# Kernel optimization log

Hardware: AMD Instinct MI355X
Metric: run time of the kernel (lower is better)

Reference implementation:

```python
import jax, jax.numpy as jnp
import numpy as np

N, L, S, C, H = 4, 2048, 4096, 256, 8
D = C // H          # head dim = 32
HID = 4 * C         # mlp hidden = 1024
LN_EPS = 1e-5
LA_EPS = 1e-6


def _layer_norm(x, g, b):
    m = x.mean(-1, keepdims=True)
    v = ((x - m) ** 2).mean(-1, keepdims=True)
    return (x - m) * jax.lax.rsqrt(v + LN_EPS) * g + b


def _linear_attention(q, k, v):
    # q: [N,L,H,D], k/v: [N,S,H,D]  (elu feature map linear attention)
    Q = jax.nn.elu(q) + 1.0
    K = jax.nn.elu(k) + 1.0
    v_len = v.shape[1]
    KV = jnp.einsum('nshd,nshv->nhdv', K, v / v_len)
    Z = 1.0 / (jnp.einsum('nlhd,nhd->nlh', Q, K.sum(axis=1)) + LA_EPS)
    return jnp.einsum('nlhd,nhdv,nlh->nlhv', Q, KV, Z) * v_len


def setup_inputs() -> dict:
    key = jax.random.key(0)
    ks = jax.random.split(key, 32)
    f32 = jnp.float32
    w = lambda k, *s: (jax.random.normal(k, s, dtype=f32) * 0.02)
    inp = {
        'tgt': jax.random.normal(ks[0], (N, L, C), dtype=f32),
        'memory': jax.random.normal(ks[1], (N, S, C), dtype=f32),
        'tgt_pos': jax.random.normal(ks[2], (N, L, C), dtype=f32),
        'pos_embed': w(ks[3], 1, S, C),
        # layer norms
        'ln1_g': jnp.ones((C,), f32), 'ln1_b': jnp.zeros((C,), f32),
        'ln2_g': jnp.ones((C,), f32), 'ln2_b': jnp.zeros((C,), f32),
        'ln3_g': jnp.ones((C,), f32), 'ln3_b': jnp.zeros((C,), f32),
        # self-attn projections (stored (in,out))
        'wq': w(ks[4], C, C), 'bq': jnp.zeros((C,), f32),
        'wk': w(ks[5], C, C), 'bk': jnp.zeros((C,), f32),
        'wv': w(ks[6], C, C), 'bv': jnp.zeros((C,), f32),
        'w_merge': w(ks[7], C, C),
        # cross-attn (CCAttention) projections
        'cwq': w(ks[8], C, C), 'cbq': jnp.zeros((C,), f32),
        'cwk': w(ks[9], C, C), 'cbk': jnp.zeros((C,), f32),
        'cwv': w(ks[10], C, C), 'cbv': jnp.zeros((C,), f32),
        'cwo': w(ks[11], C, C), 'cbo': jnp.zeros((C,), f32),
        # mlp (fc1 -> dwconv3x3 -> gelu -> fc2)
        'mw1': w(ks[12], C, HID), 'mb1': jnp.zeros((HID,), f32),
        'dw_k': w(ks[13], HID, 1, 3, 3), 'dw_b': jnp.zeros((HID,), f32),
        'mw2': w(ks[14], HID, C), 'mb2': jnp.zeros((C,), f32),
        'num_points': L,
    }
    return inp


def reference(tgt, memory, tgt_pos, pos_embed,
              ln1_g, ln1_b, ln2_g, ln2_b, ln3_g, ln3_b,
              wq, bq, wk, bk, wv, bv, w_merge,
              cwq, cbq, cwk, cbk, cwv, cbv, cwo, cbo,
              mw1, mb1, dw_k, dw_b, mw2, mb2, num_points):
    n, l, c = tgt.shape
    # ---- self attention (linear attention) ----
    tgt2 = _layer_norm(tgt, ln1_g, ln1_b)
    qk = tgt2 + tgt_pos
    q = (qk @ wq + bq).reshape(n, l, H, D)
    k = (qk @ wk + bk).reshape(n, l, H, D)
    v = (tgt2 @ wv + bv).reshape(n, l, H, D)
    msg = _linear_attention(q, k, v).reshape(n, l, c) @ w_merge
    tgt = tgt + msg  # dropout is identity in eval
    # ---- cross attention (CCAttention, softmax MHA) ----
    tgt2 = _layer_norm(tgt, ln2_g, ln2_b)
    mem = memory + pos_embed
    cq = (tgt2 @ cwq + cbq).reshape(n, l, H, D)
    ck = (mem @ cwk + cbk).reshape(n, -1, H, D)
    cv = (mem @ cwv + cbv).reshape(n, -1, H, D)
    scale = D ** -0.5
    attn = jax.nn.softmax(jnp.einsum('nlhd,nshd->nhls', cq, ck) * scale, axis=-1)
    cmsg = jnp.einsum('nhls,nshd->nlhd', attn, cv).reshape(n, l, c) @ cwo + cbo
    tgt = tgt + cmsg
    # ---- MLP with depthwise conv over (num_points, 1) grid ----
    x = _layer_norm(tgt, ln3_g, ln3_b)
    h = x @ mw1 + mb1                                   # [n,l,HID]
    hi = h.transpose(0, 2, 1).reshape(n, HID, num_points, 1)
    hi = jax.lax.conv_general_dilated(
        hi, dw_k, window_strides=(1, 1), padding=((1, 1), (1, 1)),
        feature_group_count=HID,
        dimension_numbers=('NCHW', 'OIHW', 'NCHW'))
    hi = hi + dw_b[None, :, None, None]
    h = hi.reshape(n, HID, l).transpose(0, 2, 1)
    h = jax.nn.gelu(h, approximate=False)
    mlp_out = h @ mw2 + mb2
    return tgt + mlp_out
```

## Files before the change

kernel.cpp:

```cpp
#include <hip/hip_runtime.h>
#include <hip/hip_bf16.h>
#include <math.h>

#define NB 4
#define LL 2048
#define SS 4096
#define CC 256
#define HH 8
#define DD 32
#define HIDN 1024
#define NSPLIT 2

using bf16 = __hip_bfloat16;
typedef __attribute__((ext_vector_type(8))) short short8;
typedef __attribute__((ext_vector_type(4))) short short4v;
typedef __attribute__((ext_vector_type(4))) float floatx4;

__device__ __forceinline__ float b2f(bf16 x) { return __bfloat162float(x); }
__device__ __forceinline__ short f2bs(float x) {
    bf16 h = __float2bfloat16(x);
    return *(short*)&h;
}
__device__ __forceinline__ short f2bs_fast(float x) {
    return (short)(__float_as_uint(x) >> 16);
}
__device__ __forceinline__ float s2f(short s) {
    bf16 h = *(bf16*)&s;
    return __bfloat162float(h);
}

#if __has_builtin(__builtin_amdgcn_exp2f)
#define EXP2(x) __builtin_amdgcn_exp2f(x)
#else
#define EXP2(x) exp2f(x)
#endif

__device__ __forceinline__ bool probe_f32(const unsigned* p) {
    return p[0] == 0x3F800000u;
}
__device__ __forceinline__ float ldx(const void* p, size_t i, bool f32m) {
    return f32m ? ((const float*)p)[i] : b2f(((const bf16*)p)[i]);
}

__global__ __launch_bounds__(256)
void zero_kernel(float* __restrict__ p, int n) {
    int i = blockIdx.x * 256 + threadIdx.x;
    if (i < n) p[i] = 0.0f;
}

struct WPack { const void* p[10]; };

__global__ __launch_bounds__(256)
void wprep_kernel(WPack pk, short* __restrict__ dst,
                  const unsigned* __restrict__ probe) {
    const bool f32m = probe_f32(probe);
    const int z = blockIdx.z;
    const int K = (z == 9) ? 1024 : 256;
    const int N = (z == 8) ? 1024 : 256;
    const size_t off = (z < 8) ? (size_t)z * 65536 : (z == 8 ? 524288u : 786432u);
    const int k0 = blockIdx.y * 64, n0 = blockIdx.x * 64;
    if (k0 >= K || n0 >= N) return;
    __shared__ float T[64][65];
    const void* src = pk.p[z];
    const int tid = threadIdx.x;
    #pragma unroll
    for (int p = 0; p < 16; ++p) {
        int idx = tid + p * 256;
        int r = idx >> 6, c = idx & 63;
        T[r][c] = ldx(src, (size_t)(k0 + r) * N + n0 + c, f32m);
    }
    __syncthreads();
    short* d = dst + off;
    #pragma unroll
    for (int p = 0; p < 16; ++p) {
        int idx = tid + p * 256;
        int c2 = idx >> 6, r2 = idx & 63;
        d[(size_t)(n0 + c2) * K + k0 + r2] = f2bs(T[r2][c2]);
    }
}

__global__ __launch_bounds__(256)
void ln_kernel(const void* __restrict__ xr, const float* __restrict__ xf,
               const void* __restrict__ g, const void* __restrict__ bta,
               const void* __restrict__ pos,
               short* __restrict__ y, short* __restrict__ y2,
               const unsigned* __restrict__ probe) {
    const bool f32m = probe_f32(probe);
    const int row = blockIdx.x;
    const int c = threadIdx.x;
    const size_t base = (size_t)row * CC;
    float x = xr ? ldx(xr, base + c, f32m) : xf[base + c];
    float a = x, b = x * x;
    #pragma unroll
    for (int off = 32; off; off >>= 1) {
        a += __shfl_down(a, off);
        b += __shfl_down(b, off);
    }
    __shared__ float sa[4], sb[4];
    if ((c & 63) == 0) { sa[c >> 6] = a; sb[c >> 6] = b; }
    __syncthreads();
    float s1 = sa[0] + sa[1] + sa[2] + sa[3];
    float s2 = sb[0] + sb[1] + sb[2] + sb[3];
    float mean = s1 * (1.0f / CC);
    float var = s2 * (1.0f / CC) - mean * mean;
    float inv = rsqrtf(var + 1e-5f);
    float yv = (x - mean) * inv * ldx(g, c, f32m) + ldx(bta, c, f32m);
    y[base + c] = f2bs(yv);
    if (y2) y2[base + c] = f2bs(yv + ldx(pos, base + c, f32m));
}

__global__ __launch_bounds__(256)
void addpos_kernel(const void* __restrict__ mem, const void* __restrict__ pos,
                   short* __restrict__ out, const unsigned* __restrict__ probe) {
    const bool f32m = probe_f32(probe);
    const int row = blockIdx.x;
    const int c = threadIdx.x;
    const int s = row & (SS - 1);
    out[(size_t)row * CC + c] =
        f2bs(ldx(mem, (size_t)row * CC + c, f32m) + ldx(pos, (size_t)s * CC + c, f32m));
}

template <int BM, int BN, int EPI, int OUTMODE, int TRANSC2>
__global__ __launch_bounds__(256)
void gemm_mfma_kernel(const short* __restrict__ A, const short* __restrict__ Bt,
                      const void* __restrict__ bias, const void* __restrict__ bias2,
                      const float* __restrict__ residF, const void* __restrict__ residR,
                      void* __restrict__ Cout, void* __restrict__ Cout2,
                      int M, int N, int K, const unsigned* __restrict__ probe) {
    const bool f32m = probe_f32(probe);
    constexpr int WM = BM / 2, AI = WM / 16;
    constexpr int WN = BN / 2, BJ = WN / 16;
    constexpr int ACH = (BM == 128) ? 4 : 2;
    constexpr int BCH = (BN == 128) ? 4 : 2;
    __shared__ __attribute__((aligned(16))) short As[BM][72];
    __shared__ __attribute__((aligned(16))) short Bs[BN][72];
    const int tid = threadIdx.x;
    const int ln = tid & 15, quad = (tid >> 4) & 3, w = tid >> 6;
    const int wm = (w & 1) * WM, wn = (w >> 1) * WN;
    const int bm = blockIdx.y * BM, bn = blockIdx.x * BN;
    const int ar = (BM == 128) ? (tid >> 1) : (tid >> 2);
    const int ac = (BM == 128) ? ((tid & 1) * 32) : ((tid & 3) * 16);
    const int br = (BN == 128) ? (tid >> 1) : (tid >> 2);
    const int bc = (BN == 128) ? ((tid & 1) * 32) : ((tid & 3) * 16);

    short8 pa[ACH], pb[BCH];
    {
        const short* ag = &A[(size_t)(bm + ar) * K + ac];
        #pragma unroll
        for (int t = 0; t < ACH; ++t) pa[t] = *(const short8*)(ag + t * 8);
        const short* bg = &Bt[(size_t)(bn + br) * K + bc];
        #pragma unroll
        for (int t = 0; t < BCH; ++t) pb[t] = *(const short8*)(bg + t * 8);
    }
    floatx4 acc[AI][BJ] = {};
    for (int k0 = 0; k0 < K; k0 += 64) {
        #pragma unroll
        for (int t = 0; t < ACH; ++t) *(short8*)&As[ar][ac + t * 8] = pa[t];
        #pragma unroll
        for (int t = 0; t < BCH; ++t) *(short8*)&Bs[br][bc + t * 8] = pb[t];
        if (k0 + 64 < K) {
            const short* ag = &A[(size_t)(bm + ar) * K + k0 + 64 + ac];
            #pragma unroll
            for (int t = 0; t < ACH; ++t) pa[t] = *(const short8*)(ag + t * 8);
            const short* bg = &Bt[(size_t)(bn + br) * K + k0 + 64 + bc];
            #pragma unroll
            for (int t = 0; t < BCH; ++t) pb[t] = *(const short8*)(bg + t * 8);
        }
        __syncthreads();
        #pragma unroll
        for (int ks = 0; ks < 2; ++ks) {
            short8 af[AI], bf[BJ];
            #pragma unroll
            for (int i = 0; i < AI; ++i)
                af[i] = *(const short8*)&As[wm + i * 16 + ln][ks * 32 + quad * 8];
            #pragma unroll
            for (int j = 0; j < BJ; ++j)
                bf[j] = *(const short8*)&Bs[wn + j * 16 + ln][ks * 32 + quad * 8];
            #pragma unroll
            for (int i = 0; i < AI; ++i)
                #pragma unroll
                for (int j = 0; j < BJ; ++j)
                    acc[i][j] = __builtin_amdgcn_mfma_f32_16x16x32_bf16(af[i], bf[j], acc[i][j], 0, 0, 0);
        }
        __syncthreads();
    }
    #pragma unroll
    for (int i = 0; i < AI; ++i)
        #pragma unroll
        for (int j = 0; j < BJ; ++j) {
            const int gr0 = bm + wm + i * 16 + quad * 4;
            const int gc = bn + wn + j * 16 + ln;
            const bool hi = (Cout2 != nullptr) && (gc >= 256);
            const int col = hi ? gc - 256 : gc;
            const int sN = Cout2 ? 256 : N;
            void* co = hi ? Cout2 : Cout;
            const void* bb = hi ? bias2 : bias;
            float vv[4];
            #pragma unroll
            for (int r = 0; r < 4; ++r) {
                float v = acc[i][j][r];
                if (bb) v += ldx(bb, col, f32m);
                if (EPI == 1) v = (v > 0.0f) ? (v + 1.0f) : __expf(v);
                const size_t o = (size_t)(gr0 + r) * sN + col;
                if (residF) v += residF[o];
                if (residR) v += ldx(residR, o, f32m);
                vv[r] = v;
            }
            if (TRANSC2 && hi) {
                const int nb = gr0 >> 12;
                const int s = gr0 & (SS - 1);
                short4v pk4 = {f2bs(vv[0]), f2bs(vv[1]), f2bs(vv[2]), f2bs(vv[3])};
                *(short4v*)&((short*)co)[((size_t)nb * CC + col) * SS + s] = pk4;
            } else {
                #pragma unroll
                for (int r = 0; r < 4; ++r) {
                    const size_t o = (size_t)(gr0 + r) * sN + col;
                    if (OUTMODE == 0) ((float*)co)[o] = vv[r];
                    else if (OUTMODE == 2) ((short*)co)[o] = f2bs(vv[r]);
                    else {
                        if (f32m) ((float*)co)[o] = vv[r];
                        else      ((bf16*)co)[o] = __float2bfloat16(vv[r]);
                    }
                }
            }
        }
}

#define KVSPLIT 16
__global__ __launch_bounds__(256)
void linattn_kv_kernel(const float* __restrict__ Kp, const float* __restrict__ Vp,
                       float* __restrict__ KV, float* __restrict__ Ksum) {
    const int h = blockIdx.x, n = blockIdx.y, z = blockIdx.z;
    __shared__ __attribute__((aligned(16))) float Kt[64][33];
    __shared__ __attribute__((aligned(16))) float Vt[64][32];
    const int tid = threadIdx.x;
    const int d = tid >> 3, e0 = (tid & 7) * 4;
    const int sbeg = z * (LL / KVSPLIT), send = sbeg + (LL / KVSPLIT);
    float acc[4] = {}, ks = 0.0f;
    for (int s0 = sbeg; s0 < send; s0 += 64) {
        #pragma unroll
        for (int p = 0; p < 8; ++p) {
            int idx = tid + p * 256;
            int r = idx >> 5, c = idx & 31;
            size_t gaddr = (size_t)((n * LL) + s0 + r) * CC + h * DD + c;
            Kt[r][c] = Kp[gaddr];
            Vt[r][c] = Vp[gaddr];
        }
        __syncthreads();
        for (int s = 0; s < 64; ++s) {
            float kd = Kt[s][d];
            ks += kd;
            float4 v4 = *(const float4*)&Vt[s][e0];
            acc[0] += kd * v4.x; acc[1] += kd * v4.y;
            acc[2] += kd * v4.z; acc[3] += kd * v4.w;
        }
        __syncthreads();
    }
    float* kvp = &KV[(size_t)((n * HH + h) * DD + d) * DD + e0];
    atomicAdd(&kvp[0], acc[0]); atomicAdd(&kvp[1], acc[1]);
    atomicAdd(&kvp[2], acc[2]); atomicAdd(&kvp[3], acc[3]);
    if ((tid & 7) == 0) atomicAdd(&Ksum[(n * HH + h) * DD + d], ks);
}

__global__ __launch_bounds__(256)
void linattn_out_kernel(const float* __restrict__ Qp, const float* __restrict__ KV,
                        const float* __restrict__ Ksum, short* __restrict__ Out) {
    const int lt = blockIdx.x, h = blockIdx.y, n = blockIdx.z;
    __shared__ float KVs[32][33];
    __shared__ float Ks[32];
    __shared__ float Qs[64][33];
    const int tid = threadIdx.x;
    for (int p = 0; p < 4; ++p) {
        int idx = tid + p * 256;
        KVs[idx >> 5][idx & 31] = KV[(size_t)(n * HH + h) * (DD * DD) + idx];
    }
    if (tid < 32) Ks[tid] = Ksum[(n * HH + h) * DD + tid];
    for (int p = 0; p < 8; ++p) {
        int idx = tid + p * 256;
        int r = idx >> 5, c = idx & 31;
        Qs[r][c] = Qp[(size_t)((n * LL) + lt * 64 + r) * CC + h * DD + c];
    }
    __syncthreads();
    const int e = tid & 31;
    for (int ii = 0; ii < 8; ++ii) {
        const int i = (tid >> 5) + ii * 8;
        float num = 0.0f, den = 0.0f;
        for (int d = 0; d < 32; ++d) {
            float q = Qs[i][d];
            num += q * KVs[d][e];
            den += q * Ks[d];
        }
        Out[(size_t)((n * LL) + lt * 64 + i) * CC + h * DD + e] = f2bs(num / (den + 1e-6f));
    }
}

__global__ __launch_bounds__(256)
void flash_mfma_kernel(const short* __restrict__ Q, const short* __restrict__ K,
                       const short* __restrict__ V,
                       float* __restrict__ Of, float* __restrict__ Lp) {
    const int lt = blockIdx.x, h = blockIdx.y;
    const int n = blockIdx.z >> 1, sp = blockIdx.z & 1;
    const int tid = threadIdx.x;
    const int ln = tid & 15;
    const int quad = (tid >> 4) & 3;
    const int w = tid >> 6;
    const int NT = NB * LL;
    const float qscale = 0.17677669529663687f * 1.4426950408889634f;

    __shared__ __attribute__((aligned(16))) short Qs[64][40];
    __shared__ __attribute__((aligned(16))) short Ks[64][40];
    __shared__ __attribute__((aligned(16))) short Vp[32][72];

    {
        const int r = tid >> 2, c0 = (tid & 3) * 8;
        short8 qv = *(const short8*)&Q[(size_t)((n * LL) + lt * 64 + r) * CC + h * DD + c0];
        short tmp[8];
        #pragma unroll
        for (int j = 0; j < 8; ++j) tmp[j] = f2bs(s2f(qv[j]) * qscale);
        *(short8*)&Qs[r][c0] = *(short8*)tmp;
    }
    __syncthreads();

    short8 bQ = *(const short8*)&Qs[w * 16 + ln][quad * 8];

    float l_sum = 0.0f;
    floatx4 o0 = {0.f, 0.f, 0.f, 0.f};
    floatx4 o1 = {0.f, 0.f, 0.f, 0.f};
    const floatx4 zinit = {-24.f, -24.f, -24.f, -24.f};

    const int r_st = tid >> 2, c0_st = (tid & 3) * 8;
    const int e_st = tid >> 3, m_st = tid & 7;
    const int K32 = (m_st >> 2) * 32;
    const int h4 = ((m_st >> 1) & 1) * 4;
    const int q0s = (2 * m_st) & 3;
    const int slotA = K32 + q0s * 8 + h4;
    const int slotB = K32 + (q0s + 1) * 8 + h4;

    const int sbeg = sp * (SS / NSPLIT), send = sbeg + (SS / NSPLIT);
    for (int s0 = sbeg; s0 < send; s0 += 64) {
        *(short8*)&Ks[r_st][c0_st] =
            *(const short8*)&K[(size_t)((n * SS) + s0 + r_st) * CC + h * DD + c0_st];
        {
            short8 vv = *(const short8*)&V[((size_t)n * CC + h * DD + e_st) * SS + s0 + m_st * 8];
            short4v lo = {vv[0], vv[1], vv[2], vv[3]};
            short4v hi = {vv[4], vv[5], vv[6], vv[7]};
            *(short4v*)&Vp[e_st][slotA] = lo;
            *(short4v*)&Vp[e_st][slotB] = hi;
        }
        __syncthreads();

        floatx4 sc[4];
        #pragma unroll
        for (int g = 0; g < 4; ++g) {
            short8 aK = *(const short8*)&Ks[g * 16 + ln][quad * 8];
            sc[g] = __builtin_amdgcn_mfma_f32_16x16x32_bf16(aK, bQ, zinit, 0, 0, 0);
        }

        #pragma unroll
        for (int ks = 0; ks < 2; ++ks) {
            short tmp[8];
            #pragma unroll
            for (int j = 0; j < 8; ++j) {
                float p = EXP2(sc[2 * ks + (j >> 2)][j & 3]);
                l_sum += p;
                tmp[j] = f2bs_fast(p);
            }
            short8 aP = *(short8*)tmp;
            short8 bV0 = *(const short8*)&Vp[ln][ks * 32 + quad * 8];
            short8 bV1 = *(const short8*)&Vp[16 + ln][ks * 32 + quad * 8];
            o0 = __builtin_amdgcn_mfma_f32_16x16x32_bf16(aP, bV0, o0, 0, 0, 0);
            o1 = __builtin_amdgcn_mfma_f32_16x16x32_bf16(aP, bV1, o1, 0, 0, 0);
        }
        __syncthreads();
    }

    float s = l_sum;
    s += __shfl_xor(s, 16);
    s += __shfl_xor(s, 32);
    const int rowbase = lt * 64 + w * 16;
    if (quad == 0)
        Lp[((size_t)sp * NT + (size_t)n * LL + rowbase + ln) * HH + h] = s;
    #pragma unroll
    for (int r = 0; r < 4; ++r) {
        const size_t row = (size_t)n * LL + rowbase + quad * 4 + r;
        float* o = &Of[((size_t)sp * NT + row) * CC + h * DD];
        o[ln] = o0[r];
        o[16 + ln] = o1[r];
    }
}

__global__ __launch_bounds__(256)
void flash_merge_kernel(const float* __restrict__ Of, const float* __restrict__ Lp,
                        short* __restrict__ O) {
    const int row = blockIdx.x, c = threadIdx.x, h = c >> 5;
    const size_t NT = (size_t)NB * LL;
    float l = Lp[(size_t)row * HH + h] + Lp[(NT + row) * HH + h];
    float v = Of[(size_t)row * CC + c] + Of[NT * CC + (size_t)row * CC + c];
    O[(size_t)row * CC + c] = f2bs(v / l);
}

__global__ __launch_bounds__(256)
void dwconv_gelu_kernel(const short* __restrict__ H1, const void* __restrict__ wk,
                        const void* __restrict__ wb, short* __restrict__ H2,
                        const unsigned* __restrict__ probe) {
    const bool f32m = probe_f32(probe);
    const int row = blockIdx.x;
    const int l = row & (LL - 1);
    const int c0 = threadIdx.x * 4;
    const short* cur = &H1[(size_t)row * HIDN + c0];
    short4v xc = *(const short4v*)cur;
    short4v xm = {}, xp = {};
    if (l > 0)      xm = *(const short4v*)(cur - HIDN);
    if (l < LL - 1) xp = *(const short4v*)(cur + HIDN);
    short r[4];
    #pragma unroll
    for (int j = 0; j < 4; ++j) {
        int ch = c0 + j;
        float wm = ldx(wk, ch * 9 + 1, f32m);
        float w0 = ldx(wk, ch * 9 + 4, f32m);
        float wp = ldx(wk, ch * 9 + 7, f32m);
        float v = s2f(xm[j]) * wm + s2f(xc[j]) * w0 + s2f(xp[j]) * wp + ldx(wb, ch, f32m);
        r[j] = f2bs(0.5f * v * (1.0f + erff(v * 0.70710678118654752f)));
    }
    short4v out = {r[0], r[1], r[2], r[3]};
    *(short4v*)&H2[(size_t)row * HIDN + c0] = out;
}

extern "C" void kernel_launch(void* const* d_in, const int* in_sizes, int n_in,
                              void* d_out, int out_size, void* d_ws, size_t ws_size,
                              hipStream_t stream) {
    const void* tgt      = d_in[0];
    const void* memory   = d_in[1];
    const void* tgt_pos  = d_in[2];
    const void* pos_emb  = d_in[3];
    const void* ln1_g = d_in[4],  *ln1_b = d_in[5];
    const void* ln2_g = d_in[6],  *ln2_b = d_in[7];
    const void* ln3_g = d_in[8],  *ln3_b = d_in[9];
    const void* wq = d_in[10], *bq = d_in[11];
    const void* wk = d_in[12], *bk = d_in[13];
    const void* wv = d_in[14], *bv = d_in[15];
    const void* w_merge = d_in[16];
    const void* cwq = d_in[17], *cbq = d_in[18];
    const void* cwk = d_in[19], *cbk = d_in[20];
    const void* cwv = d_in[21], *cbv = d_in[22];
    const void* cwo = d_in[23], *cbo = d_in[24];
    const void* mw1 = d_in[25], *mb1 = d_in[26];
    const void* dw_k = d_in[27], *dw_b = d_in[28];
    const void* mw2 = d_in[29], *mb2 = d_in[30];
    const unsigned* probe = (const unsigned*)d_in[4];

    char* w = (char*)d_ws;
    const size_t MB = 1024 * 1024;
    short* lnout_b = (short*)(w + 0 * MB);
    short* qk_b    = (short*)(w + 4 * MB);
    float* Tbuf    = (float*)(w + 8 * MB);
    float* phiq    = (float*)(w + 16 * MB);
    float* phik    = (float*)(w + 24 * MB);
    float* vbuf    = (float*)(w + 32 * MB);
    float* KVb     = (float*)(w + 40 * MB);
    float* Ksb     = (float*)(w + 40 * MB + 131072);
    short* cqbuf   = (short*)(w + 41 * MB);
    short* membuf  = (short*)(w + 45 * MB);
    short* ckbuf   = (short*)(w + 53 * MB);
    short* cvT     = (short*)(w + 69 * MB);
    short* flashO  = (short*)(w + 77 * MB);
    short* wT      = (short*)(w + 81 * MB);
    float* Ofb     = (float*)(w + 16 * MB);
    float* Lpb     = (float*)(w + 32 * MB);
    short* H1      = (short*)(w + 16 * MB);
    short* H2      = (short*)(w + 32 * MB);

    short* wqT  = wT + 0 * 65536;
    short* wvT  = wT + 2 * 65536;
    short* wmT  = wT + 3 * 65536;
    short* cwqT = wT + 4 * 65536;
    short* cwkT = wT + 5 * 65536;
    short* cwoT = wT + 7 * 65536;
    short* mw1T = wT + 524288;
    short* mw2T = wT + 786432;

    const int NT = NB * LL;
    const int NS = NB * SS;
    const dim3 blk(256);

    WPack pk;
    pk.p[0] = wq;  pk.p[1] = wk;  pk.p[2] = wv;  pk.p[3] = w_merge;
    pk.p[4] = cwq; pk.p[5] = cwk; pk.p[6] = cwv; pk.p[7] = cwo;
    pk.p[8] = mw1; pk.p[9] = mw2;
    wprep_kernel<<<dim3(16, 16, 10), blk, 0, stream>>>(pk, wT, probe);
    zero_kernel<<<dim3(137), blk, 0, stream>>>(KVb, 35072);

    ln_kernel<<<NT, blk, 0, stream>>>(tgt, nullptr, ln1_g, ln1_b, tgt_pos, lnout_b, qk_b, probe);
    gemm_mfma_kernel<64, 64, 1, 0, 0><<<dim3(8, NT / 64), blk, 0, stream>>>(
        qk_b, wqT, bq, bk, nullptr, nullptr, phiq, phik, NT, 512, CC, probe);
    gemm_mfma_kernel<64, 64, 0, 0, 0><<<dim3(4, NT / 64), blk, 0, stream>>>(
        lnout_b, wvT, bv, nullptr, nullptr, nullptr, vbuf, nullptr, NT, CC, CC, probe);
    linattn_kv_kernel<<<dim3(HH, NB, KVSPLIT), blk, 0, stream>>>(phik, vbuf, KVb, Ksb);
    linattn_out_kernel<<<dim3(LL / 64, HH, NB), blk, 0, stream>>>(phiq, KVb, Ksb, (short*)vbuf);
    gemm_mfma_kernel<64, 64, 0, 0, 0><<<dim3(4, NT / 64), blk, 0, stream>>>(
        (short*)vbuf, wmT, nullptr, nullptr, nullptr, tgt, Tbuf, nullptr, NT, CC, CC, probe);

    ln_kernel<<<NT, blk, 0, stream>>>(nullptr, Tbuf, ln2_g, ln2_b, nullptr, lnout_b, nullptr, probe);
    addpos_kernel<<<NS, blk, 0, stream>>>(memory, pos_emb, membuf, probe);
    gemm_mfma_kernel<64, 64, 0, 2, 0><<<dim3(4, NT / 64), blk, 0, stream>>>(
        lnout_b, cwqT, cbq, nullptr, nullptr, nullptr, cqbuf, nullptr, NT, CC, CC, probe);
    gemm_mfma_kernel<64, 64, 0, 2, 1><<<dim3(8, NS / 64), blk, 0, stream>>>(
        membuf, cwkT, cbk, cbv, nullptr, nullptr, ckbuf, cvT, NS, 512, CC, probe);
    flash_mfma_kernel<<<dim3(LL / 64, HH, NB * NSPLIT), blk, 0, stream>>>(
        cqbuf, ckbuf, cvT, Ofb, Lpb);
    flash_merge_kernel<<<NT, blk, 0, stream>>>(Ofb, Lpb, flashO);
    gemm_mfma_kernel<64, 64, 0, 0, 0><<<dim3(4, NT / 64), blk, 0, stream>>>(
        flashO, cwoT, cbo, nullptr, Tbuf, nullptr, Tbuf, nullptr, NT, CC, CC, probe);

    ln_kernel<<<NT, blk, 0, stream>>>(nullptr, Tbuf, ln3_g, ln3_b, nullptr, lnout_b, nullptr, probe);
    gemm_mfma_kernel<64, 64, 0, 2, 0><<<dim3(16, NT / 64), blk, 0, stream>>>(
        lnout_b, mw1T, mb1, nullptr, nullptr, nullptr, H1, nullptr, NT, HIDN, CC, probe);
    dwconv_gelu_kernel<<<NT, blk, 0, stream>>>(H1, dw_k, dw_b, H2, probe);
    gemm_mfma_kernel<64, 64, 0, 1, 0><<<dim3(4, NT / 64), blk, 0, stream>>>(
        H2, mw2T, mb2, nullptr, Tbuf, nullptr, d_out, nullptr, NT, CC, HIDN, probe);

    (void)in_sizes; (void)n_in; (void)out_size; (void)ws_size;
}
```

Measured before the change: 425.4 us.

## Load GEMM tiles straight into LDS with global_load_lds and enlarge tiles

```diff
diff --git a/kernel.cpp b/kernel.cpp
--- a/kernel.cpp
+++ b/kernel.cpp
@@ -34,6 +34,12 @@
 #else
 #define EXP2(x) exp2f(x)
 #endif
+
+__device__ __forceinline__ void gload16(const void* g, void* l) {
+    __builtin_amdgcn_global_load_lds(
+        (const __attribute__((address_space(1))) void*)g,
+        (__attribute__((address_space(3))) void*)l, 16, 0, 0);
+}
 
 __device__ __forceinline__ bool probe_f32(const unsigned* p) {
     return p[0] == 0x3F800000u;
@@ -130,41 +136,26 @@
     const bool f32m = probe_f32(probe);
     constexpr int WM = BM / 2, AI = WM / 16;
     constexpr int WN = BN / 2, BJ = WN / 16;
-    constexpr int ACH = (BM == 128) ? 4 : 2;
-    constexpr int BCH = (BN == 128) ? 4 : 2;
-    __shared__ __attribute__((aligned(16))) short As[BM][72];
-    __shared__ __attribute__((aligned(16))) short Bs[BN][72];
+    __shared__ __attribute__((aligned(16))) short As[BM][64];
+    __shared__ __attribute__((aligned(16))) short Bs[BN][64];
     const int tid = threadIdx.x;
     const int ln = tid & 15, quad = (tid >> 4) & 3, w = tid >> 6;
     const int wm = (w & 1) * WM, wn = (w >> 1) * WN;
     const int bm = blockIdx.y * BM, bn = blockIdx.x * BN;
-    const int ar = (BM == 128) ? (tid >> 1) : (tid >> 2);
-    const int ac = (BM == 128) ? ((tid & 1) * 32) : ((tid & 3) * 16);
-    const int br = (BN == 128) ? (tid >> 1) : (tid >> 2);
-    const int bc = (BN == 128) ? ((tid & 1) * 32) : ((tid & 3) * 16);
-
-    short8 pa[ACH], pb[BCH];
-    {
-        const short* ag = &A[(size_t)(bm + ar) * K + ac];
-        #pragma unroll
-        for (int t = 0; t < ACH; ++t) pa[t] = *(const short8*)(ag + t * 8);
-        const short* bg = &Bt[(size_t)(bn + br) * K + bc];
-        #pragma unroll
-        for (int t = 0; t < BCH; ++t) pb[t] = *(const short8*)(bg + t * 8);
-    }
+    const int l64 = tid & 63;
+    const int srow = l64 >> 3, scol = (l64 & 7) * 8;
+
     floatx4 acc[AI][BJ] = {};
     for (int k0 = 0; k0 < K; k0 += 64) {
         #pragma unroll
-        for (int t = 0; t < ACH; ++t) *(short8*)&As[ar][ac + t * 8] = pa[t];
-        #pragma unroll
-        for (int t = 0; t < BCH; ++t) *(short8*)&Bs[br][bc + t * 8] = pb[t];
-        if (k0 + 64 < K) {
-            const short* ag = &A[(size_t)(bm + ar) * K + k0 + 64 + ac];
-            #pragma unroll
-            for (int t = 0; t < ACH; ++t) pa[t] = *(const short8*)(ag + t * 8);
-            const short* bg = &Bt[(size_t)(bn + br) * K + k0 + 64 + bc];
-            #pragma unroll
-            for (int t = 0; t < BCH; ++t) pb[t] = *(const short8*)(bg + t * 8);
+        for (int t = 0; t < BM / 32; ++t) {
+            const int r = (t * 4 + w) * 8 + srow;
+            gload16(&A[(size_t)(bm + r) * K + k0 + scol], &As[r][scol]);
+        }
+        #pragma unroll
+        for (int t = 0; t < BN / 32; ++t) {
+            const int r = (t * 4 + w) * 8 + srow;
+            gload16(&Bt[(size_t)(bn + r) * K + k0 + scol], &Bs[r][scol]);
         }
         __syncthreads();
         #pragma unroll
@@ -491,7 +482,7 @@
     zero_kernel<<<dim3(137), blk, 0, stream>>>(KVb, 35072);
 
     ln_kernel<<<NT, blk, 0, stream>>>(tgt, nullptr, ln1_g, ln1_b, tgt_pos, lnout_b, qk_b, probe);
-    gemm_mfma_kernel<64, 64, 1, 0, 0><<<dim3(8, NT / 64), blk, 0, stream>>>(
+    gemm_mfma_kernel<128, 64, 1, 0, 0><<<dim3(8, NT / 128), blk, 0, stream>>>(
         qk_b, wqT, bq, bk, nullptr, nullptr, phiq, phik, NT, 512, CC, probe);
     gemm_mfma_kernel<64, 64, 0, 0, 0><<<dim3(4, NT / 64), blk, 0, stream>>>(
         lnout_b, wvT, bv, nullptr, nullptr, nullptr, vbuf, nullptr, NT, CC, CC, probe);
@@ -504,7 +495,7 @@
     addpos_kernel<<<NS, blk, 0, stream>>>(memory, pos_emb, membuf, probe);
     gemm_mfma_kernel<64, 64, 0, 2, 0><<<dim3(4, NT / 64), blk, 0, stream>>>(
         lnout_b, cwqT, cbq, nullptr, nullptr, nullptr, cqbuf, nullptr, NT, CC, CC, probe);
-    gemm_mfma_kernel<64, 64, 0, 2, 1><<<dim3(8, NS / 64), blk, 0, stream>>>(
+    gemm_mfma_kernel<128, 128, 0, 2, 1><<<dim3(4, NS / 128), blk, 0, stream>>>(
         membuf, cwkT, cbk, cbv, nullptr, nullptr, ckbuf, cvT, NS, 512, CC, probe);
     flash_mfma_kernel<<<dim3(LL / 64, HH, NB * NSPLIT), blk, 0, stream>>>(
         cqbuf, ckbuf, cvT, Ofb, Lpb);
@@ -513,7 +504,7 @@
         flashO, cwoT, cbo, nullptr, Tbuf, nullptr, Tbuf, nullptr, NT, CC, CC, probe);
 
     ln_kernel<<<NT, blk, 0, stream>>>(nullptr, Tbuf, ln3_g, ln3_b, nullptr, lnout_b, nullptr, probe);
-    gemm_mfma_kernel<64, 64, 0, 2, 0><<<dim3(16, NT / 64), blk, 0, stream>>>(
+    gemm_mfma_kernel<128, 128, 0, 2, 0><<<dim3(8, NT / 128), blk, 0, stream>>>(
         lnout_b, mw1T, mb1, nullptr, nullptr, nullptr, H1, nullptr, NT, HIDN, CC, probe);
     dwconv_gelu_kernel<<<NT, blk, 0, stream>>>(H1, dw_k, dw_b, H2, probe);
     gemm_mfma_kernel<64, 64, 0, 1, 0><<<dim3(4, NT / 64), blk, 0, stream>>>(
```

Result: slower. 543.8 us (+27.8%).
